# Performance work log

Hardware: AMD Instinct MI355X
Metric: run time of the kernel (lower is better)

## Reference

```python
import jax, jax.numpy as jnp
import numpy as np

E = 8        # n_experts
K = 2        # top-k
DIM = 1024
HID = 2048   # swiglu hidden; fc1 out = 2*HID
B, T = 4, 2048


def setup_inputs() -> dict:
    key = jax.random.key(0)
    ks = jax.random.split(key, 7)
    s = 0.02
    return {
        "x": jax.random.normal(ks[0], (B, T, DIM), dtype=jnp.float32),
        "router_w": jax.random.normal(ks[1], (E, DIM), dtype=jnp.float32) * s,
        "router_b": jnp.zeros((E,), dtype=jnp.float32),
        "W1": jax.random.normal(ks[2], (E, DIM, 2 * HID), dtype=jnp.float32) * s,
        "b1": jnp.zeros((E, 2 * HID), dtype=jnp.float32),
        "W2": jax.random.normal(ks[3], (E, HID, DIM), dtype=jnp.float32) * s,
        "b2": jnp.zeros((E, DIM), dtype=jnp.float32),
    }


def _swiglu(h):
    h1, h2 = jnp.split(h, 2, axis=-1)
    return jax.nn.silu(h1) * h2


def reference(x, router_w, router_b, W1, b1, W2, b2):
    # Router: logits = Linear(dim, E), temperature = 1.0
    logits = jnp.einsum("btd,ed->bte", x, router_w) + router_b  # [B,T,E]
    topk_val, topk_idx = jax.lax.top_k(logits, K)               # [B,T,K]
    weights = jax.nn.softmax(topk_val, axis=-1)                 # softmax router
    # combine[b,t,e] = sum_k weights[b,t,k] * [topk_idx[b,t,k] == e]
    combine = jnp.sum(jax.nn.one_hot(topk_idx, E, dtype=x.dtype)
                      * weights[..., None], axis=-2)            # [B,T,E]
    out = jnp.zeros_like(x)
    # Fixed small loop over experts (structurally distinct weight slices).
    for e in range(E):
        h = jnp.einsum("btd,dh->bth", x, W1[e]) + b1[e]         # [B,T,2H]
        y = jnp.einsum("bth,hd->btd", _swiglu(h), W2[e]) + b2[e]
        out = out + combine[..., e:e + 1] * y
    return out
```

## Files before the change

kernel.cpp:

```cpp
#include <hip/hip_runtime.h>
#include <stdint.h>

typedef unsigned short u16;

#define E_    8
#define DIM_  1024
#define HID_  2048
#define H2_   4096
#define NTOK  8192
#define RTOK  32

typedef __attribute__((ext_vector_type(8))) short bf16x8;
typedef __attribute__((ext_vector_type(4))) float f32x4;

__device__ __forceinline__ u16 f2bf(float f) {
  uint32_t u = __builtin_bit_cast(uint32_t, f);
  uint32_t r = (u + 0x7FFFu + ((u >> 16) & 1u)) >> 16;
  return (u16)r;
}
__device__ __forceinline__ float bf2f(u16 u) {
  return __builtin_bit_cast(float, (uint32_t)u << 16);
}

__device__ __forceinline__ void gload16(const void* g, void* l) {
  __builtin_amdgcn_global_load_lds(
      (const __attribute__((address_space(1))) void*)g,
      (__attribute__((address_space(3))) void*)l, 16, 0, 0);
}


__global__ void cvt_x(const float* __restrict__ x, u16* __restrict__ xb, int n8) {
  int i = blockIdx.x * blockDim.x + threadIdx.x;
  if (i >= n8) return;
  const float4* p = (const float4*)(x + (size_t)i * 8);
  float4 a = p[0], b = p[1];
  union { u16 u[8]; uint4 v; } r;
  r.u[0] = f2bf(a.x); r.u[1] = f2bf(a.y); r.u[2] = f2bf(a.z); r.u[3] = f2bf(a.w);
  r.u[4] = f2bf(b.x); r.u[5] = f2bf(b.y); r.u[6] = f2bf(b.z); r.u[7] = f2bf(b.w);
  *(uint4*)(xb + (size_t)i * 8) = r.v;
}

__global__ void tconv(const float* __restrict__ src, u16* __restrict__ dst, int R, int C) {
  __shared__ float t[32][33];
  int e = blockIdx.z;
  int r0 = blockIdx.y * 32, c0 = blockIdx.x * 32;
  const float* s = src + (size_t)e * R * C;
  u16* d = dst + (size_t)e * R * C;
  int tid = threadIdx.x;
  int rr = tid >> 3, cc = (tid & 7) * 4;
  float4 v = *(const float4*)(s + (size_t)(r0 + rr) * C + c0 + cc);
  t[rr][cc + 0] = v.x; t[rr][cc + 1] = v.y; t[rr][cc + 2] = v.z; t[rr][cc + 3] = v.w;
  __syncthreads();
  ushort4 w;
  w.x = f2bf(t[cc + 0][rr]);
  w.y = f2bf(t[cc + 1][rr]);
  w.z = f2bf(t[cc + 2][rr]);
  w.w = f2bf(t[cc + 3][rr]);
  *(ushort4*)(d + (size_t)(c0 + rr) * R + r0 + cc) = w;
}


__global__ void router(const float* __restrict__ x, const float* __restrict__ rw,
                       const float* __restrict__ rb, int* __restrict__ counts,
                       int* __restrict__ btok, float* __restrict__ bw,
                       int* __restrict__ tokrec) {
  __shared__ float srw[E_ * DIM_];
  __shared__ float sb[E_];
  __shared__ int   hcnt[E_], hbase[E_];
  __shared__ int   te[RTOK * 2];
  __shared__ float twt[RTOK * 2];
  __shared__ int   tloc[RTOK * 2];

  int tid = threadIdx.x;
  for (int i = tid; i < E_ * DIM_ / 4; i += 256)
    ((float4*)srw)[i] = ((const float4*)rw)[i];
  if (tid < E_) { sb[tid] = rb[tid]; hcnt[tid] = 0; }
  __syncthreads();

  int wid = tid >> 6, lane = tid & 63;
#pragma unroll
  for (int s = 0; s < RTOK / 4; ++s) {
    int lt = wid * (RTOK / 4) + s;
    int t = blockIdx.x * RTOK + lt;
    const float* xt = x + (size_t)t * DIM_;
    float acc[8] = {0.f, 0.f, 0.f, 0.f, 0.f, 0.f, 0.f, 0.f};
#pragma unroll
    for (int it = 0; it < 4; ++it) {
      int d = it * 256 + lane * 4;
      float4 xv = *(const float4*)(xt + d);
#pragma unroll
      for (int e = 0; e < 8; ++e) {
        float4 rv = *(const float4*)(&srw[e * DIM_ + d]);
        acc[e] += xv.x * rv.x + xv.y * rv.y + xv.z * rv.z + xv.w * rv.w;
      }
    }
#pragma unroll
    for (int e = 0; e < 8; ++e)
#pragma unroll
      for (int off = 32; off; off >>= 1)
        acc[e] += __shfl_xor(acc[e], off, 64);
    if (lane == 0) {
      float v[8];
#pragma unroll
      for (int e = 0; e < 8; ++e) v[e] = acc[e] + sb[e];
      int i0 = 0;
#pragma unroll
      for (int e = 1; e < 8; ++e) if (v[e] > v[i0]) i0 = e;
      int i1 = (i0 == 0) ? 1 : 0;
#pragma unroll
      for (int e = 0; e < 8; ++e) if (e != i0 && v[e] > v[i1]) i1 = e;
      float w0 = 1.f / (1.f + expf(v[i1] - v[i0]));
      float w1 = 1.f - w0;
      int l0 = atomicAdd(&hcnt[i0], 1);
      int l1 = atomicAdd(&hcnt[i1], 1);
      te[lt * 2 + 0] = i0; twt[lt * 2 + 0] = w0; tloc[lt * 2 + 0] = l0;
      te[lt * 2 + 1] = i1; twt[lt * 2 + 1] = w1; tloc[lt * 2 + 1] = l1;
    }
  }
  __syncthreads();
  if (tid < E_) hbase[tid] = atomicAdd(&counts[tid], hcnt[tid]);
  __syncthreads();
  if (tid < RTOK * 2) {
    int e = te[tid];
    int p = hbase[e] + tloc[tid];
    int t = blockIdx.x * RTOK + (tid >> 1);
    btok[e * NTOK + p] = t;
    bw[e * NTOK + p] = twt[tid];
    tokrec[t * 2 + (tid & 1)] = (e << 13) | p;
  }
}


__launch_bounds__(256, 2)
__global__ void gemm1(const u16* __restrict__ xb, const u16* __restrict__ w1t,
                      const float* __restrict__ b1, const int* __restrict__ counts,
                      const int* __restrict__ btok, u16* __restrict__ hb) {
  int e = blockIdx.z, mblk = blockIdx.y, nblk = blockIdx.x;
  int cnt = counts[e];
  if (mblk * 128 >= cnt) return;
  int base = 0;
#pragma unroll
  for (int i = 0; i < 8; ++i) base += (i < e) ? counts[i] : 0;

  __shared__ u16 lA[128 * 64];
  __shared__ u16 lB[128 * 64];
  __shared__ int sTok[128];

  int tid = threadIdx.x, wid = tid >> 6, lane = tid & 63;
  if (tid < 128) {
    int gr = mblk * 128 + tid;
    sTok[tid] = (gr < cnt) ? btok[e * NTOK + gr] : btok[e * NTOK];
  }
  __syncthreads();

  f32x4 acc[4][4] = {};
  int wr = wid >> 1, wc = wid & 1;
  int l15 = lane & 15, lhi = lane >> 4;
  const size_t w1e = (size_t)e * H2_ * DIM_;

  int segsw = ((lane & 7) ^ ((lane >> 3) & 7)) * 8;
  const u16* gA[4];
  const u16* gB[4];
#pragma unroll
  for (int i = 0; i < 4; ++i) {
    int r = wid * 32 + i * 8 + (lane >> 3);
    gA[i] = xb + (size_t)sTok[r] * DIM_ + segsw;
    int gcol = nblk * 64 + (r >> 6) * 32 + (r & 31) + ((r >> 5) & 1) * 2048;
    gB[i] = w1t + w1e + (size_t)gcol * DIM_ + segsw;
  }
  int rxor = (l15 & 7) * 8;

  for (int kt = 0; kt < DIM_ / 64; ++kt) {
#pragma unroll
    for (int i = 0; i < 4; ++i)
      gload16(gA[i] + kt * 64, &lA[(wid * 32 + i * 8) * 64]);
#pragma unroll
    for (int i = 0; i < 4; ++i)
      gload16(gB[i] + kt * 64, &lB[(wid * 32 + i * 8) * 64]);
    __syncthreads();
#pragma unroll
    for (int ks = 0; ks < 2; ++ks) {
      int segrd = ((ks * 4 + lhi) * 8) ^ rxor;
      bf16x8 a[4], b[4];
#pragma unroll
      for (int m = 0; m < 4; ++m)
        a[m] = *(const bf16x8*)&lA[(wr * 64 + m * 16 + l15) * 64 + segrd];
#pragma unroll
      for (int n = 0; n < 4; ++n)
        b[n] = *(const bf16x8*)&lB[(wc * 64 + n * 16 + l15) * 64 + segrd];
#pragma unroll
      for (int m = 0; m < 4; ++m)
#pragma unroll
        for (int n = 0; n < 4; ++n)
          acc[m][n] = __builtin_amdgcn_mfma_f32_16x16x32_bf16(a[m], b[n], acc[m][n], 0, 0, 0);
    }
    __syncthreads();
  }

#pragma unroll
  for (int n = 0; n < 2; ++n) {
    int outcol = nblk * 64 + wc * 32 + n * 16 + l15;
    float bb1 = b1[e * H2_ + outcol];
    float bb2 = b1[e * H2_ + outcol + HID_];
#pragma unroll
    for (int m = 0; m < 4; ++m) {
#pragma unroll
      for (int j = 0; j < 4; ++j) {
        int rt = wr * 64 + m * 16 + lhi * 4 + j;
        int gr = mblk * 128 + rt;
        if (gr < cnt) {
          float h1 = acc[m][n][j] + bb1;
          float h2 = acc[m][n + 2][j] + bb2;
          float s = (h1 / (1.f + __expf(-h1))) * h2;
          hb[(size_t)(base + gr) * HID_ + outcol] = f2bf(s);
        }
      }
    }
  }
}


__launch_bounds__(256, 2)
__global__ void gemm2(const u16* __restrict__ hb, const u16* __restrict__ w2t,
                      const float* __restrict__ b2, const int* __restrict__ counts,
                      const float* __restrict__ bw, u16* __restrict__ ybuf) {
  int e = blockIdx.z, mblk = blockIdx.y, nblk = blockIdx.x;
  int cnt = counts[e];
  if (mblk * 128 >= cnt) return;
  int base = 0;
#pragma unroll
  for (int i = 0; i < 8; ++i) base += (i < e) ? counts[i] : 0;

  __shared__ u16 lA[128 * 64];
  __shared__ u16 lB[128 * 64];
  __shared__ float sW[128];

  int tid = threadIdx.x, wid = tid >> 6, lane = tid & 63;
  if (tid < 128) {
    int gr = mblk * 128 + tid;
    sW[tid] = (gr < cnt) ? bw[e * NTOK + gr] : 0.f;
  }
  __syncthreads();

  f32x4 acc[4][4] = {};
  int wr = wid >> 1, wc = wid & 1;
  int l15 = lane & 15, lhi = lane >> 4;

  int segsw = ((lane & 7) ^ ((lane >> 3) & 7)) * 8;
  const u16* gA[4];
  const u16* gB[4];
#pragma unroll
  for (int i = 0; i < 4; ++i) {
    int r = wid * 32 + i * 8 + (lane >> 3);
    gA[i] = hb + (size_t)(base + mblk * 128 + r) * HID_ + segsw;
    gB[i] = w2t + (size_t)e * DIM_ * HID_ + (size_t)(nblk * 128 + r) * HID_ + segsw;
  }
  int rxor = (l15 & 7) * 8;

  for (int kt = 0; kt < HID_ / 64; ++kt) {
#pragma unroll
    for (int i = 0; i < 4; ++i) {
      gload16(gA[i] + kt * 64, &lA[(wid * 32 + i * 8) * 64]);
      gload16(gB[i] + kt * 64, &lB[(wid * 32 + i * 8) * 64]);
    }
    __syncthreads();
#pragma unroll
    for (int ks = 0; ks < 2; ++ks) {
      int segrd = ((ks * 4 + lhi) * 8) ^ rxor;
      bf16x8 a[4], b[4];
#pragma unroll
      for (int m = 0; m < 4; ++m)
        a[m] = *(const bf16x8*)&lA[(wr * 64 + m * 16 + l15) * 64 + segrd];
#pragma unroll
      for (int n = 0; n < 4; ++n)
        b[n] = *(const bf16x8*)&lB[(wc * 64 + n * 16 + l15) * 64 + segrd];
#pragma unroll
      for (int m = 0; m < 4; ++m)
#pragma unroll
        for (int n = 0; n < 4; ++n)
          acc[m][n] = __builtin_amdgcn_mfma_f32_16x16x32_bf16(a[m], b[n], acc[m][n], 0, 0, 0);
    }
    __syncthreads();
  }

#pragma unroll
  for (int n = 0; n < 4; ++n) {
    int col = nblk * 128 + wc * 64 + n * 16 + l15;
    float bb = b2[e * DIM_ + col];
#pragma unroll
    for (int m = 0; m < 4; ++m) {
#pragma unroll
      for (int j = 0; j < 4; ++j) {
        int rt = wr * 64 + m * 16 + lhi * 4 + j;
        int gr = mblk * 128 + rt;
        if (gr < cnt)
          ybuf[(size_t)(base + gr) * DIM_ + col] = f2bf(sW[rt] * (acc[m][n][j] + bb));
      }
    }
  }
}


__global__ void combine(const u16* __restrict__ ybuf, const int* __restrict__ tokrec,
                        const int* __restrict__ counts, float* __restrict__ out) {
  __shared__ int sbase[8];
  int tid = threadIdx.x;
  if (tid == 0) {
    int b = 0;
#pragma unroll
    for (int e = 0; e < 8; ++e) { sbase[e] = b; b += counts[e]; }
  }
  __syncthreads();
  int t = blockIdx.x;
  int r0 = tokrec[t * 2 + 0], r1 = tokrec[t * 2 + 1];
  size_t s0 = (size_t)(sbase[r0 >> 13] + (r0 & 8191)) * DIM_;
  size_t s1 = (size_t)(sbase[r1 >> 13] + (r1 & 8191)) * DIM_;
  int c = tid * 4;
  ushort4 a = *(const ushort4*)(ybuf + s0 + c);
  ushort4 b = *(const ushort4*)(ybuf + s1 + c);
  float4 o;
  o.x = bf2f(a.x) + bf2f(b.x);
  o.y = bf2f(a.y) + bf2f(b.y);
  o.z = bf2f(a.z) + bf2f(b.z);
  o.w = bf2f(a.w) + bf2f(b.w);
  *(float4*)(out + (size_t)t * DIM_ + c) = o;
}


extern "C" void kernel_launch(void* const* d_in, const int* in_sizes, int n_in,
                              void* d_out, int out_size, void* d_ws, size_t ws_size,
                              hipStream_t stream) {
  const float* x  = (const float*)d_in[0];
  const float* rw = (const float*)d_in[1];
  const float* rb = (const float*)d_in[2];
  const float* W1 = (const float*)d_in[3];
  const float* b1 = (const float*)d_in[4];
  const float* W2 = (const float*)d_in[5];
  const float* b2 = (const float*)d_in[6];
  float* out = (float*)d_out;

  char* ws = (char*)d_ws;
  int*   counts = (int*)ws;
  int*   btok   = (int*)(ws + 256);
  float* bw     = (float*)(ws + 256 + 262144);
  int*   tokrec = (int*)(ws + 256 + 524288);
  u16* xb  = (u16*)(ws + (1u << 20));
  u16* w1t = xb  + (size_t)NTOK * DIM_;
  u16* w2t = w1t + (size_t)E_ * H2_ * DIM_;
  u16* hb  = w2t + (size_t)E_ * DIM_ * HID_;
  u16* ybuf = w1t;

  hipMemsetAsync(counts, 0, 8 * sizeof(int), stream);

  cvt_x<<<(NTOK * DIM_ / 8 + 255) / 256, 256, 0, stream>>>(x, xb, NTOK * DIM_ / 8);
  tconv<<<dim3(H2_ / 32, DIM_ / 32, E_), 256, 0, stream>>>(W1, w1t, DIM_, H2_);
  tconv<<<dim3(DIM_ / 32, HID_ / 32, E_), 256, 0, stream>>>(W2, w2t, HID_, DIM_);
  router<<<NTOK / RTOK, 256, 0, stream>>>(x, rw, rb, counts, btok, bw, tokrec);

  gemm1<<<dim3(H2_ / 128, NTOK / 128, E_), 256, 0, stream>>>(xb, w1t, b1, counts, btok, hb);
  gemm2<<<dim3(DIM_ / 128, NTOK / 128, E_), 256, 0, stream>>>(hb, w2t, b2, counts, bw, ybuf);
  combine<<<NTOK, 256, 0, stream>>>(ybuf, tokrec, counts, out);
}
```

Baseline: 403.4 us.

## Use 256x256 tiles with 8 waves and double-buffered LDS pipeline in expert GEMMs

Both expert GEMMs move from 128x128 tiles with 4 waves and a single LDS buffer to 256x256 tiles with 8 waves and a two-stage LDS ring (128 KB). Global-to-LDS loads for upcoming k-tiles are interleaved with MFMA work on the current ones, using fine-grained barriers, vmcnt waits and s_setprio. The aim is to hide memory latency and raise operand reuse per loaded byte. In exchange, the LDS footprint limits occupancy, larger tiles waste more work on partial expert row blocks, and the synchronisation is intricate.

```diff
diff --git a/kernel.cpp b/kernel.cpp
--- a/kernel.cpp
+++ b/kernel.cpp
@@ -9,6 +9,8 @@
 #define H2_   4096
 #define NTOK  8192
 #define RTOK  32
+#define NT1   16
+#define NT2   32
 
 typedef __attribute__((ext_vector_type(8))) short bf16x8;
 typedef __attribute__((ext_vector_type(4))) float f32x4;
@@ -131,88 +133,125 @@
 }
 
 
-__launch_bounds__(256, 2)
+#define STG2(sm_, pArr, buf, reg, half, tile, NTt)                         \
+  {                                                                        \
+    int tc_ = (tile) < (NTt) ? (tile) : (NTt)-1;                           \
+    u16* d_ = (sm_) + (buf)*32768 + (reg)*16384 + (half)*8192 + wid * 512; \
+    gload16(pArr[(half)*2 + 0] + tc_ * 64, d_);                            \
+    gload16(pArr[(half)*2 + 1] + tc_ * 64, d_ + 4096);                     \
+  }
+
+
+__launch_bounds__(512, 2)
 __global__ void gemm1(const u16* __restrict__ xb, const u16* __restrict__ w1t,
                       const float* __restrict__ b1, const int* __restrict__ counts,
                       const int* __restrict__ btok, u16* __restrict__ hb) {
   int e = blockIdx.z, mblk = blockIdx.y, nblk = blockIdx.x;
   int cnt = counts[e];
-  if (mblk * 128 >= cnt) return;
+  if (mblk * 256 >= cnt) return;
   int base = 0;
 #pragma unroll
   for (int i = 0; i < 8; ++i) base += (i < e) ? counts[i] : 0;
 
-  __shared__ u16 lA[128 * 64];
-  __shared__ u16 lB[128 * 64];
-  __shared__ int sTok[128];
+  __shared__ u16 sm[65536];
+  __shared__ int sTok[256];
 
   int tid = threadIdx.x, wid = tid >> 6, lane = tid & 63;
-  if (tid < 128) {
-    int gr = mblk * 128 + tid;
+  if (tid < 256) {
+    int gr = mblk * 256 + tid;
     sTok[tid] = (gr < cnt) ? btok[e * NTOK + gr] : btok[e * NTOK];
   }
   __syncthreads();
 
-  f32x4 acc[4][4] = {};
-  int wr = wid >> 1, wc = wid & 1;
+  int wr = wid >> 2, wc = wid & 3;
   int l15 = lane & 15, lhi = lane >> 4;
+  int rxor = (l15 & 7) * 8;
+  int segsw = ((tid & 7) ^ ((tid >> 3) & 7)) * 8;
+  int rowi = tid >> 3;
+
+  const u16* pA[4];
+  const u16* pB[4];
   const size_t w1e = (size_t)e * H2_ * DIM_;
-
-  int segsw = ((lane & 7) ^ ((lane >> 3) & 7)) * 8;
-  const u16* gA[4];
-  const u16* gB[4];
-#pragma unroll
-  for (int i = 0; i < 4; ++i) {
-    int r = wid * 32 + i * 8 + (lane >> 3);
-    gA[i] = xb + (size_t)sTok[r] * DIM_ + segsw;
-    int gcol = nblk * 64 + (r >> 6) * 32 + (r & 31) + ((r >> 5) & 1) * 2048;
-    gB[i] = w1t + w1e + (size_t)gcol * DIM_ + segsw;
-  }
-  int rxor = (l15 & 7) * 8;
-
-  for (int kt = 0; kt < DIM_ / 64; ++kt) {
-#pragma unroll
-    for (int i = 0; i < 4; ++i)
-      gload16(gA[i] + kt * 64, &lA[(wid * 32 + i * 8) * 64]);
-#pragma unroll
-    for (int i = 0; i < 4; ++i)
-      gload16(gB[i] + kt * 64, &lB[(wid * 32 + i * 8) * 64]);
-    __syncthreads();
-#pragma unroll
-    for (int ks = 0; ks < 2; ++ks) {
-      int segrd = ((ks * 4 + lhi) * 8) ^ rxor;
-      bf16x8 a[4], b[4];
-#pragma unroll
-      for (int m = 0; m < 4; ++m)
-        a[m] = *(const bf16x8*)&lA[(wr * 64 + m * 16 + l15) * 64 + segrd];
-#pragma unroll
-      for (int n = 0; n < 4; ++n)
-        b[n] = *(const bf16x8*)&lB[(wc * 64 + n * 16 + l15) * 64 + segrd];
-#pragma unroll
-      for (int m = 0; m < 4; ++m)
-#pragma unroll
-        for (int n = 0; n < 4; ++n)
-          acc[m][n] = __builtin_amdgcn_mfma_f32_16x16x32_bf16(a[m], b[n], acc[m][n], 0, 0, 0);
-    }
-    __syncthreads();
-  }
-
-#pragma unroll
-  for (int n = 0; n < 2; ++n) {
-    int outcol = nblk * 64 + wc * 32 + n * 16 + l15;
-    float bb1 = b1[e * H2_ + outcol];
-    float bb2 = b1[e * H2_ + outcol + HID_];
-#pragma unroll
-    for (int m = 0; m < 4; ++m) {
+#pragma unroll
+  for (int j = 0; j < 4; ++j) {
+    int r = j * 64 + rowi;
+    pA[j] = xb + (size_t)sTok[r] * DIM_ + segsw;
+    int gcol = nblk * 128 + j * 32 + (rowi & 31) + ((rowi >> 5) & 1) * 2048;
+    pB[j] = w1t + w1e + (size_t)gcol * DIM_ + segsw;
+  }
+
+  STG2(sm, pA, 0, 0, 0, 0, NT1); STG2(sm, pA, 0, 0, 1, 0, NT1);
+  STG2(sm, pB, 0, 1, 0, 0, NT1); STG2(sm, pB, 0, 1, 1, 0, NT1);
+  STG2(sm, pA, 1, 0, 0, 1, NT1); STG2(sm, pA, 1, 0, 1, 1, NT1);
+  asm volatile("s_waitcnt vmcnt(4)" ::: "memory");
+  __builtin_amdgcn_s_barrier();
+
+  f32x4 acc[8][4] = {};
+
+  for (int i = 0; i < NT1 / 2; ++i) {
+    int t2 = 2 * i;
+#pragma unroll
+    for (int h = 0; h < 2; ++h) {
+      u16* A = sm + h * 32768;
+      u16* B = A + 16384;
+      bf16x8 a[8][2];
+#pragma unroll
+      for (int q = 0; q < 4; ++q) {
+        if (q == 0) {
+#pragma unroll
+          for (int m = 0; m < 8; ++m)
+#pragma unroll
+            for (int kk = 0; kk < 2; ++kk)
+              a[m][kk] = *(const bf16x8*)&A[(wr * 128 + m * 16 + l15) * 64 +
+                                            (((kk * 4 + lhi) * 8) ^ rxor)];
+        }
+        int brow = (wc * 64 + q * 16 + l15) * 64;
+        bf16x8 b0 = *(const bf16x8*)&B[brow + ((lhi * 8) ^ rxor)];
+        bf16x8 b1f = *(const bf16x8*)&B[brow + (((4 + lhi) * 8) ^ rxor)];
+        if (h == 0) {
+          if (q == 0)      STG2(sm, pB, 1, 1, 0, t2 + 1, NT1)
+          else if (q == 1) STG2(sm, pB, 1, 1, 1, t2 + 1, NT1)
+          else if (q == 2) STG2(sm, pA, 0, 0, 0, t2 + 2, NT1)
+          else             STG2(sm, pA, 0, 0, 1, t2 + 2, NT1)
+        } else {
+          if (q == 0)      STG2(sm, pB, 0, 1, 0, t2 + 2, NT1)
+          else if (q == 1) STG2(sm, pB, 0, 1, 1, t2 + 2, NT1)
+          else if (q == 2) STG2(sm, pA, 1, 0, 0, t2 + 3, NT1)
+          else             STG2(sm, pA, 1, 0, 1, t2 + 3, NT1)
+        }
+        asm volatile("" ::: "memory");
+        __builtin_amdgcn_s_barrier();
+        __builtin_amdgcn_s_setprio(1);
+#pragma unroll
+        for (int m = 0; m < 8; ++m) {
+          acc[m][q] = __builtin_amdgcn_mfma_f32_16x16x32_bf16(a[m][0], b0, acc[m][q], 0, 0, 0);
+          acc[m][q] = __builtin_amdgcn_mfma_f32_16x16x32_bf16(a[m][1], b1f, acc[m][q], 0, 0, 0);
+        }
+        __builtin_amdgcn_s_setprio(0);
+        if (q == 3) asm volatile("s_waitcnt vmcnt(4)" ::: "memory");
+        asm volatile("" ::: "memory");
+        __builtin_amdgcn_s_barrier();
+      }
+    }
+  }
+  asm volatile("s_waitcnt vmcnt(0)" ::: "memory");
+
+#pragma unroll
+  for (int q = 0; q < 2; ++q) {
+    int oc = nblk * 128 + wc * 32 + q * 16 + l15;
+    float bb1 = b1[e * H2_ + oc];
+    float bb2 = b1[e * H2_ + oc + HID_];
+#pragma unroll
+    for (int m = 0; m < 8; ++m) {
 #pragma unroll
       for (int j = 0; j < 4; ++j) {
-        int rt = wr * 64 + m * 16 + lhi * 4 + j;
-        int gr = mblk * 128 + rt;
+        int rt = wr * 128 + m * 16 + lhi * 4 + j;
+        int gr = mblk * 256 + rt;
         if (gr < cnt) {
-          float h1 = acc[m][n][j] + bb1;
-          float h2 = acc[m][n + 2][j] + bb2;
+          float h1 = acc[m][q][j] + bb1;
+          float h2 = acc[m][q + 2][j] + bb2;
           float s = (h1 / (1.f + __expf(-h1))) * h2;
-          hb[(size_t)(base + gr) * HID_ + outcol] = f2bf(s);
+          hb[(size_t)(base + gr) * HID_ + oc] = f2bf(s);
         }
       }
     }
@@ -220,81 +259,110 @@
 }
 
 
-__launch_bounds__(256, 2)
+__launch_bounds__(512, 2)
 __global__ void gemm2(const u16* __restrict__ hb, const u16* __restrict__ w2t,
                       const float* __restrict__ b2, const int* __restrict__ counts,
                       const float* __restrict__ bw, u16* __restrict__ ybuf) {
   int e = blockIdx.z, mblk = blockIdx.y, nblk = blockIdx.x;
   int cnt = counts[e];
-  if (mblk * 128 >= cnt) return;
+  if (mblk * 256 >= cnt) return;
   int base = 0;
 #pragma unroll
   for (int i = 0; i < 8; ++i) base += (i < e) ? counts[i] : 0;
 
-  __shared__ u16 lA[128 * 64];
-  __shared__ u16 lB[128 * 64];
-  __shared__ float sW[128];
+  __shared__ u16 sm[65536];
+  __shared__ float sW[256];
 
   int tid = threadIdx.x, wid = tid >> 6, lane = tid & 63;
-  if (tid < 128) {
-    int gr = mblk * 128 + tid;
+  if (tid < 256) {
+    int gr = mblk * 256 + tid;
     sW[tid] = (gr < cnt) ? bw[e * NTOK + gr] : 0.f;
   }
   __syncthreads();
 
-  f32x4 acc[4][4] = {};
-  int wr = wid >> 1, wc = wid & 1;
+  int wr = wid >> 2, wc = wid & 3;
   int l15 = lane & 15, lhi = lane >> 4;
-
-  int segsw = ((lane & 7) ^ ((lane >> 3) & 7)) * 8;
-  const u16* gA[4];
-  const u16* gB[4];
-#pragma unroll
-  for (int i = 0; i < 4; ++i) {
-    int r = wid * 32 + i * 8 + (lane >> 3);
-    gA[i] = hb + (size_t)(base + mblk * 128 + r) * HID_ + segsw;
-    gB[i] = w2t + (size_t)e * DIM_ * HID_ + (size_t)(nblk * 128 + r) * HID_ + segsw;
-  }
   int rxor = (l15 & 7) * 8;
-
-  for (int kt = 0; kt < HID_ / 64; ++kt) {
-#pragma unroll
-    for (int i = 0; i < 4; ++i) {
-      gload16(gA[i] + kt * 64, &lA[(wid * 32 + i * 8) * 64]);
-      gload16(gB[i] + kt * 64, &lB[(wid * 32 + i * 8) * 64]);
-    }
-    __syncthreads();
-#pragma unroll
-    for (int ks = 0; ks < 2; ++ks) {
-      int segrd = ((ks * 4 + lhi) * 8) ^ rxor;
-      bf16x8 a[4], b[4];
-#pragma unroll
-      for (int m = 0; m < 4; ++m)
-        a[m] = *(const bf16x8*)&lA[(wr * 64 + m * 16 + l15) * 64 + segrd];
-#pragma unroll
-      for (int n = 0; n < 4; ++n)
-        b[n] = *(const bf16x8*)&lB[(wc * 64 + n * 16 + l15) * 64 + segrd];
-#pragma unroll
-      for (int m = 0; m < 4; ++m)
-#pragma unroll
-        for (int n = 0; n < 4; ++n)
-          acc[m][n] = __builtin_amdgcn_mfma_f32_16x16x32_bf16(a[m], b[n], acc[m][n], 0, 0, 0);
-    }
-    __syncthreads();
-  }
-
-#pragma unroll
-  for (int n = 0; n < 4; ++n) {
-    int col = nblk * 128 + wc * 64 + n * 16 + l15;
+  int segsw = ((tid & 7) ^ ((tid >> 3) & 7)) * 8;
+  int rowi = tid >> 3;
+
+  const u16* pA[4];
+  const u16* pB[4];
+#pragma unroll
+  for (int j = 0; j < 4; ++j) {
+    pA[j] = hb + (size_t)(base + mblk * 256 + j * 64 + rowi) * HID_ + segsw;
+    pB[j] = w2t + (size_t)e * DIM_ * HID_ +
+            (size_t)(nblk * 256 + j * 64 + rowi) * HID_ + segsw;
+  }
+
+  STG2(sm, pA, 0, 0, 0, 0, NT2); STG2(sm, pA, 0, 0, 1, 0, NT2);
+  STG2(sm, pB, 0, 1, 0, 0, NT2); STG2(sm, pB, 0, 1, 1, 0, NT2);
+  STG2(sm, pA, 1, 0, 0, 1, NT2); STG2(sm, pA, 1, 0, 1, 1, NT2);
+  asm volatile("s_waitcnt vmcnt(4)" ::: "memory");
+  __builtin_amdgcn_s_barrier();
+
+  f32x4 acc[8][4] = {};
+
+  for (int i = 0; i < NT2 / 2; ++i) {
+    int t2 = 2 * i;
+#pragma unroll
+    for (int h = 0; h < 2; ++h) {
+      u16* A = sm + h * 32768;
+      u16* B = A + 16384;
+      bf16x8 a[8][2];
+#pragma unroll
+      for (int q = 0; q < 4; ++q) {
+        if (q == 0) {
+#pragma unroll
+          for (int m = 0; m < 8; ++m)
+#pragma unroll
+            for (int kk = 0; kk < 2; ++kk)
+              a[m][kk] = *(const bf16x8*)&A[(wr * 128 + m * 16 + l15) * 64 +
+                                            (((kk * 4 + lhi) * 8) ^ rxor)];
+        }
+        int brow = (wc * 64 + q * 16 + l15) * 64;
+        bf16x8 b0 = *(const bf16x8*)&B[brow + ((lhi * 8) ^ rxor)];
+        bf16x8 b1f = *(const bf16x8*)&B[brow + (((4 + lhi) * 8) ^ rxor)];
+        if (h == 0) {
+          if (q == 0)      STG2(sm, pB, 1, 1, 0, t2 + 1, NT2)
+          else if (q == 1) STG2(sm, pB, 1, 1, 1, t2 + 1, NT2)
+          else if (q == 2) STG2(sm, pA, 0, 0, 0, t2 + 2, NT2)
+          else             STG2(sm, pA, 0, 0, 1, t2 + 2, NT2)
+        } else {
+          if (q == 0)      STG2(sm, pB, 0, 1, 0, t2 + 2, NT2)
+          else if (q == 1) STG2(sm, pB, 0, 1, 1, t2 + 2, NT2)
+          else if (q == 2) STG2(sm, pA, 1, 0, 0, t2 + 3, NT2)
+          else             STG2(sm, pA, 1, 0, 1, t2 + 3, NT2)
+        }
+        asm volatile("" ::: "memory");
+        __builtin_amdgcn_s_barrier();
+        __builtin_amdgcn_s_setprio(1);
+#pragma unroll
+        for (int m = 0; m < 8; ++m) {
+          acc[m][q] = __builtin_amdgcn_mfma_f32_16x16x32_bf16(a[m][0], b0, acc[m][q], 0, 0, 0);
+          acc[m][q] = __builtin_amdgcn_mfma_f32_16x16x32_bf16(a[m][1], b1f, acc[m][q], 0, 0, 0);
+        }
+        __builtin_amdgcn_s_setprio(0);
+        if (q == 3) asm volatile("s_waitcnt vmcnt(4)" ::: "memory");
+        asm volatile("" ::: "memory");
+        __builtin_amdgcn_s_barrier();
+      }
+    }
+  }
+  asm volatile("s_waitcnt vmcnt(0)" ::: "memory");
+
+#pragma unroll
+  for (int q = 0; q < 4; ++q) {
+    int col = nblk * 256 + wc * 64 + q * 16 + l15;
     float bb = b2[e * DIM_ + col];
 #pragma unroll
-    for (int m = 0; m < 4; ++m) {
+    for (int m = 0; m < 8; ++m) {
 #pragma unroll
       for (int j = 0; j < 4; ++j) {
-        int rt = wr * 64 + m * 16 + lhi * 4 + j;
-        int gr = mblk * 128 + rt;
+        int rt = wr * 128 + m * 16 + lhi * 4 + j;
+        int gr = mblk * 256 + rt;
         if (gr < cnt)
-          ybuf[(size_t)(base + gr) * DIM_ + col] = f2bf(sW[rt] * (acc[m][n][j] + bb));
+          ybuf[(size_t)(base + gr) * DIM_ + col] = f2bf(sW[rt] * (acc[m][q][j] + bb));
       }
     }
   }
@@ -357,7 +425,7 @@
   tconv<<<dim3(DIM_ / 32, HID_ / 32, E_), 256, 0, stream>>>(W2, w2t, HID_, DIM_);
   router<<<NTOK / RTOK, 256, 0, stream>>>(x, rw, rb, counts, btok, bw, tokrec);
 
-  gemm1<<<dim3(H2_ / 128, NTOK / 128, E_), 256, 0, stream>>>(xb, w1t, b1, counts, btok, hb);
-  gemm2<<<dim3(DIM_ / 128, NTOK / 128, E_), 256, 0, stream>>>(hb, w2t, b2, counts, bw, ybuf);
+  gemm1<<<dim3(H2_ / 256, NTOK / 256, E_), 512, 0, stream>>>(xb, w1t, b1, counts, btok, hb);
+  gemm2<<<dim3(DIM_ / 256, NTOK / 256, E_), 512, 0, stream>>>(hb, w2t, b2, counts, bw, ybuf);
   combine<<<NTOK, 256, 0, stream>>>(ybuf, tokrec, counts, out);
 }
```

Result: slower. 570.5 us (+41.4%).
